# Performance work log

Hardware: AMD Instinct MI355X
Metric: run time of the kernel (lower is better)

## Reference

```python
import jax, jax.numpy as jnp
import numpy as np

T, B, I, H = 2048, 64, 256, 512

def _orthogonal(key, rows, cols):
    # mimic torch.nn.init.orthogonal_ semantics (QR of gaussian, sign-fixed)
    a = jax.random.normal(key, (max(rows, cols), min(rows, cols)), dtype=jnp.float32)
    q, r = jnp.linalg.qr(a)
    q = q * jnp.sign(jnp.diagonal(r))
    if rows < cols:
        q = q.T
    return q[:rows, :cols]

def setup_inputs() -> dict:
    key = jax.random.key(0)
    k1, k2, k3 = jax.random.split(key, 3)
    inp = jax.random.normal(k1, (T, B, I), dtype=jnp.float32)
    w_in = _orthogonal(k2, I, H)
    w_rec = _orthogonal(k3, H, H)
    return {"input": inp, "w_in": w_in, "w_rec": w_rec}

def reference(input, w_in, w_rec):
    # Precompute input projections for all timesteps in one big GEMM: [T,B,H]
    x_proj = jnp.einsum('tbi,ih->tbh', input, w_in)
    h0 = jnp.zeros((input.shape[1], w_rec.shape[0]), dtype=input.dtype)

    def step(h, xp_t):
        h_next = jnp.tanh(xp_t + h @ w_rec)
        return h_next, h_next

    h_last, hiddens = jax.lax.scan(step, h0, x_proj)
    return hiddens, h_last
```

## Files before the change

### kernel.cpp

```cpp
#include <hip/hip_runtime.h>

#define T_STEPS 2048
#define BATCH   64
#define IN_DIM  256
#define HID     512

typedef _Float16 half_t;
typedef half_t half2_t __attribute__((ext_vector_type(2)));

#if __has_builtin(__builtin_amdgcn_fdot2)
__device__ __forceinline__ float fdot2(half2_t a, half2_t b, float c) {
    return __builtin_amdgcn_fdot2(a, b, c, false);
}
#else
__device__ __forceinline__ float fdot2(half2_t a, half2_t b, float c) {
    return c + (float)a.x * (float)b.x + (float)a.y * (float)b.y;
}
#endif

struct alignas(16) h2x4 { half2_t v[4]; };

__global__ __launch_bounds__(256, 4)
void xproj_gemm(const float* __restrict__ A, const float* __restrict__ Win,
                float* __restrict__ out) {
    __shared__ float As[32][132];
    __shared__ float Bs[32][132];
    const int tid = threadIdx.x;
    const int m0 = blockIdx.y * 128;
    const int n0 = blockIdx.x * 128;
    const int tm = (tid >> 4) << 3;
    const int tn = (tid & 15) << 3;

    float acc[8][8] = {};

    for (int k0 = 0; k0 < IN_DIM; k0 += 32) {
        {
            const int m  = tid >> 3;
            const int k4 = (tid & 7) << 2;
#pragma unroll
            for (int r = 0; r < 4; ++r) {
                const float4 a4 = *(const float4*)&A[(size_t)(m0 + m + 32 * r) * IN_DIM + k0 + k4];
                As[k4 + 0][m + 32 * r] = a4.x;
                As[k4 + 1][m + 32 * r] = a4.y;
                As[k4 + 2][m + 32 * r] = a4.z;
                As[k4 + 3][m + 32 * r] = a4.w;
            }
        }
        {
            const int kb = tid >> 5;
            const int n4 = (tid & 31) << 2;
#pragma unroll
            for (int r = 0; r < 4; ++r) {
                const float4 b4 = *(const float4*)&Win[(size_t)(k0 + kb + 8 * r) * HID + n0 + n4];
                *(float4*)&Bs[kb + 8 * r][n4] = b4;
            }
        }
        __syncthreads();
#pragma unroll
        for (int kk = 0; kk < 32; ++kk) {
            const float4 a0 = *(const float4*)&As[kk][tm];
            const float4 a1 = *(const float4*)&As[kk][tm + 4];
            const float4 b0 = *(const float4*)&Bs[kk][tn];
            const float4 b1 = *(const float4*)&Bs[kk][tn + 4];
            const float av[8] = {a0.x, a0.y, a0.z, a0.w, a1.x, a1.y, a1.z, a1.w};
            const float bv[8] = {b0.x, b0.y, b0.z, b0.w, b1.x, b1.y, b1.z, b1.w};
#pragma unroll
            for (int i = 0; i < 8; ++i)
#pragma unroll
                for (int j = 0; j < 8; ++j)
                    acc[i][j] = fmaf(av[i], bv[j], acc[i][j]);
        }
        __syncthreads();
    }

#pragma unroll
    for (int i = 0; i < 8; ++i) {
        float4 c0 = {acc[i][0], acc[i][1], acc[i][2], acc[i][3]};
        float4 c1 = {acc[i][4], acc[i][5], acc[i][6], acc[i][7]};
        float* dst = &out[(size_t)(m0 + tm + i) * HID + n0 + tn];
        *(float4*)dst       = c0;
        *(float4*)(dst + 4) = c1;
    }
}

__global__ __attribute__((amdgpu_flat_work_group_size(512, 512),
                          amdgpu_waves_per_eu(2, 2)))
void rnn_scan(const float* __restrict__ Wrec, float* __restrict__ out) {
    __shared__ h2x4  WL4[16 * 512];
    __shared__ float parts[8 * 640];
    __shared__ h2x4  h4buf[64];

    const int tid   = threadIdx.x;
    const int b     = blockIdx.x;
    const int jg    = tid & 63;
    const int kg    = tid >> 6;
    const int col0  = jg << 3;
    const int kbase = kg << 6;

    half2_t wreg[8][24];
#pragma unroll
    for (int p = 0; p < 24; ++p) {
        const int k = kbase + 2 * p;
        const float4 lo0 = *(const float4*)&Wrec[(size_t)k * HID + col0];
        const float4 lo1 = *(const float4*)&Wrec[(size_t)k * HID + col0 + 4];
        const float4 hi0 = *(const float4*)&Wrec[(size_t)(k + 1) * HID + col0];
        const float4 hi1 = *(const float4*)&Wrec[(size_t)(k + 1) * HID + col0 + 4];
        wreg[0][p].x = (half_t)lo0.x; wreg[0][p].y = (half_t)hi0.x;
        wreg[1][p].x = (half_t)lo0.y; wreg[1][p].y = (half_t)hi0.y;
        wreg[2][p].x = (half_t)lo0.z; wreg[2][p].y = (half_t)hi0.z;
        wreg[3][p].x = (half_t)lo0.w; wreg[3][p].y = (half_t)hi0.w;
        wreg[4][p].x = (half_t)lo1.x; wreg[4][p].y = (half_t)hi1.x;
        wreg[5][p].x = (half_t)lo1.y; wreg[5][p].y = (half_t)hi1.y;
        wreg[6][p].x = (half_t)lo1.z; wreg[6][p].y = (half_t)hi1.z;
        wreg[7][p].x = (half_t)lo1.w; wreg[7][p].y = (half_t)hi1.w;
    }
#pragma unroll
    for (int q = 0; q < 2; ++q) {
        h2x4 bu[8];
#pragma unroll
        for (int pp = 0; pp < 4; ++pp) {
            const int k = kbase + 48 + 8 * q + 2 * pp;
            const float4 lo0 = *(const float4*)&Wrec[(size_t)k * HID + col0];
            const float4 lo1 = *(const float4*)&Wrec[(size_t)k * HID + col0 + 4];
            const float4 hi0 = *(const float4*)&Wrec[(size_t)(k + 1) * HID + col0];
            const float4 hi1 = *(const float4*)&Wrec[(size_t)(k + 1) * HID + col0 + 4];
            bu[0].v[pp].x = (half_t)lo0.x; bu[0].v[pp].y = (half_t)hi0.x;
            bu[1].v[pp].x = (half_t)lo0.y; bu[1].v[pp].y = (half_t)hi0.y;
            bu[2].v[pp].x = (half_t)lo0.z; bu[2].v[pp].y = (half_t)hi0.z;
            bu[3].v[pp].x = (half_t)lo0.w; bu[3].v[pp].y = (half_t)hi0.w;
            bu[4].v[pp].x = (half_t)lo1.x; bu[4].v[pp].y = (half_t)hi1.x;
            bu[5].v[pp].x = (half_t)lo1.y; bu[5].v[pp].y = (half_t)hi1.y;
            bu[6].v[pp].x = (half_t)lo1.z; bu[6].v[pp].y = (half_t)hi1.z;
            bu[7].v[pp].x = (half_t)lo1.w; bu[7].v[pp].y = (half_t)hi1.w;
        }
#pragma unroll
        for (int c = 0; c < 8; ++c)
            WL4[(c * 2 + q) * 512 + tid] = bu[c];
    }
    if (tid < 64) {
        h2x4 z;
        z.v[0] = half2_t{(half_t)0.f, (half_t)0.f};
        z.v[1] = z.v[0]; z.v[2] = z.v[0]; z.v[3] = z.v[0];
        h4buf[tid] = z;
    }
    __syncthreads();

    const int jcol  = tid;
    const int pbase = 9 * (jcol >> 3) + (jcol & 7);
    const h2x4* hbase = &h4buf[kg << 3];

    for (int t = 0; t < T_STEPS; ++t) {
        const float xpv = out[((size_t)t * BATCH + b) * HID + jcol];

        float acc[8] = {};

#pragma unroll
        for (int j = 0; j < 6; ++j) {
            const h2x4 hu = hbase[j];
#pragma unroll
            for (int pp = 0; pp < 4; ++pp)
#pragma unroll
                for (int c = 0; c < 8; ++c)
                    acc[c] = fdot2(wreg[c][4 * j + pp], hu.v[pp], acc[c]);
        }
#pragma unroll
        for (int q = 0; q < 2; ++q) {
            const h2x4 hu = hbase[6 + q];
#pragma unroll
            for (int c = 0; c < 8; ++c) {
                const h2x4 wu = WL4[(c * 2 + q) * 512 + tid];
#pragma unroll
                for (int pp = 0; pp < 4; ++pp)
                    acc[c] = fdot2(wu.v[pp], hu.v[pp], acc[c]);
            }
        }
#pragma unroll
        for (int c = 0; c < 8; ++c)
            parts[kg * 640 + 9 * jg + c] = acc[c];
        __syncthreads();

        float s = xpv;
#pragma unroll
        for (int g = 0; g < 8; ++g)
            s += parts[g * 640 + pbase];
        const float e  = __expf(2.0f * s);
        const float hj = 1.0f - 2.0f / (e + 1.0f);

        out[((size_t)t * BATCH + b) * HID + jcol] = hj;
        if (t == T_STEPS - 1)
            out[(size_t)T_STEPS * BATCH * HID + (size_t)b * HID + jcol] = hj;

        ((half_t*)h4buf)[jcol] = (half_t)hj;
        __syncthreads();
    }
}

extern "C" void kernel_launch(void* const* d_in, const int* in_sizes, int n_in,
                              void* d_out, int out_size, void* d_ws, size_t ws_size,
                              hipStream_t stream) {
    const float* A    = (const float*)d_in[0];
    const float* Win  = (const float*)d_in[1];
    const float* Wrec = (const float*)d_in[2];
    float* out = (float*)d_out;

    dim3 g1(HID / 128, (T_STEPS * BATCH) / 128);
    xproj_gemm<<<g1, 256, 0, stream>>>(A, Win, out);
    rnn_scan<<<BATCH, 512, 0, stream>>>(Wrec, out);
}
```

Measured before the change: 3.626 ms.

## Offload half of recurrent matvec to MFMA alongside fdot2 partial sums

The recurrent h@W_rec reduction is split in two. The upper 256 K-rows are computed with MFMA 16x16x32 f16 instructions, using B fragments held in registers and a broadcast h row, and only output row 0 is kept. The lower 256 K-rows still go through the fdot2 register/LDS path, now with half the per-thread work. The aim is to cut per-step VALU latency on the serial critical path by using the matrix cores, even though most of each MFMA tile is wasted and an extra LDS reduction buffer is added. The end-of-step __syncthreads is also replaced by an explicit lgkmcnt wait plus s_barrier.

Measured after the change: 4.620 ms. 1.27x slower.

```diff
diff --git a/kernel.cpp b/kernel.cpp
--- a/kernel.cpp
+++ b/kernel.cpp
@@ -7,6 +7,8 @@
 
 typedef _Float16 half_t;
 typedef half_t half2_t __attribute__((ext_vector_type(2)));
+typedef _Float16 f16x8 __attribute__((ext_vector_type(8)));
+typedef float f32x4 __attribute__((ext_vector_type(4)));
 
 #if __has_builtin(__builtin_amdgcn_fdot2)
 __device__ __forceinline__ float fdot2(half2_t a, half2_t b, float c) {
@@ -86,20 +88,23 @@
 __global__ __attribute__((amdgpu_flat_work_group_size(512, 512),
                           amdgpu_waves_per_eu(2, 2)))
 void rnn_scan(const float* __restrict__ Wrec, float* __restrict__ out) {
-    __shared__ h2x4  WL4[16 * 512];
+    __shared__ h2x4  WA[8 * 512];
+    __shared__ h2x4  WB[8 * 512];
     __shared__ float parts[8 * 640];
-    __shared__ h2x4  h4buf[64];
+    __shared__ float parts_m[512];
+    __shared__ f16x8 h2raw[64];
 
     const int tid   = threadIdx.x;
     const int b     = blockIdx.x;
     const int jg    = tid & 63;
     const int kg    = tid >> 6;
     const int col0  = jg << 3;
-    const int kbase = kg << 6;
-
-    half2_t wreg[8][24];
-#pragma unroll
-    for (int p = 0; p < 24; ++p) {
+    const int kbase = kg << 5;
+    const int lane  = tid & 63;
+
+    half2_t wreg[8][8];
+#pragma unroll
+    for (int p = 0; p < 8; ++p) {
         const int k = kbase + 2 * p;
         const float4 lo0 = *(const float4*)&Wrec[(size_t)k * HID + col0];
         const float4 lo1 = *(const float4*)&Wrec[(size_t)k * HID + col0 + 4];
@@ -119,7 +124,7 @@
         h2x4 bu[8];
 #pragma unroll
         for (int pp = 0; pp < 4; ++pp) {
-            const int k = kbase + 48 + 8 * q + 2 * pp;
+            const int k = kbase + 16 + 8 * q + 2 * pp;
             const float4 lo0 = *(const float4*)&Wrec[(size_t)k * HID + col0];
             const float4 lo1 = *(const float4*)&Wrec[(size_t)k * HID + col0 + 4];
             const float4 hi0 = *(const float4*)&Wrec[(size_t)(k + 1) * HID + col0];
@@ -133,53 +138,95 @@
             bu[6].v[pp].x = (half_t)lo1.z; bu[6].v[pp].y = (half_t)hi1.z;
             bu[7].v[pp].x = (half_t)lo1.w; bu[7].v[pp].y = (half_t)hi1.w;
         }
+        h2x4* slab = q ? WB : WA;
 #pragma unroll
         for (int c = 0; c < 8; ++c)
-            WL4[(c * 2 + q) * 512 + tid] = bu[c];
-    }
+            slab[c * 512 + tid] = bu[c];
+    }
+    const int lrow = tid & 15;
+    const int lgrp = (tid >> 4) & 3;
+    f16x8 bfrag[4][8];
+#pragma unroll
+    for (int tl = 0; tl < 4; ++tl)
+#pragma unroll
+        for (int K = 0; K < 8; ++K) {
+            const int col = (kg << 6) + (tl << 4) + lrow;
+            const int kb  = 256 + (K << 5) + (lgrp << 3);
+            f16x8 f;
+#pragma unroll
+            for (int i = 0; i < 8; ++i)
+                f[i] = (half_t)Wrec[(size_t)(kb + i) * HID + col];
+            bfrag[tl][K] = f;
+        }
     if (tid < 64) {
-        h2x4 z;
-        z.v[0] = half2_t{(half_t)0.f, (half_t)0.f};
-        z.v[1] = z.v[0]; z.v[2] = z.v[0]; z.v[3] = z.v[0];
-        h4buf[tid] = z;
+        f16x8 z;
+#pragma unroll
+        for (int i = 0; i < 8; ++i) z[i] = (half_t)0.f;
+        h2raw[tid] = z;
     }
     __syncthreads();
 
-    const int jcol  = tid;
-    const int pbase = 9 * (jcol >> 3) + (jcol & 7);
-    const h2x4* hbase = &h4buf[kg << 3];
+    const h2x4* hb4  = (const h2x4*)h2raw;
+    const int jcol   = tid;
+    const int pbase  = 9 * (jcol >> 3) + (jcol & 7);
 
     for (int t = 0; t < T_STEPS; ++t) {
         const float xpv = out[((size_t)t * BATCH + b) * HID + jcol];
 
+        f32x4 d0 = {0.f, 0.f, 0.f, 0.f};
+        f32x4 d1 = d0, d2 = d0, d3 = d0;
+#pragma unroll
+        for (int K = 0; K < 8; ++K) {
+            const f16x8 af = h2raw[32 + (K << 2) + lgrp];
+            d0 = __builtin_amdgcn_mfma_f32_16x16x32_f16(af, bfrag[0][K], d0, 0, 0, 0);
+            d1 = __builtin_amdgcn_mfma_f32_16x16x32_f16(af, bfrag[1][K], d1, 0, 0, 0);
+            d2 = __builtin_amdgcn_mfma_f32_16x16x32_f16(af, bfrag[2][K], d2, 0, 0, 0);
+            d3 = __builtin_amdgcn_mfma_f32_16x16x32_f16(af, bfrag[3][K], d3, 0, 0, 0);
+        }
+
         float acc[8] = {};
-
-#pragma unroll
-        for (int j = 0; j < 6; ++j) {
-            const h2x4 hu = hbase[j];
+#pragma unroll
+        for (int j = 0; j < 2; ++j) {
+            const h2x4 hu = hb4[(kg << 2) + j];
 #pragma unroll
             for (int pp = 0; pp < 4; ++pp)
 #pragma unroll
                 for (int c = 0; c < 8; ++c)
                     acc[c] = fdot2(wreg[c][4 * j + pp], hu.v[pp], acc[c]);
         }
-#pragma unroll
-        for (int q = 0; q < 2; ++q) {
-            const h2x4 hu = hbase[6 + q];
+        {
+            const h2x4 hu = hb4[(kg << 2) + 2];
 #pragma unroll
             for (int c = 0; c < 8; ++c) {
-                const h2x4 wu = WL4[(c * 2 + q) * 512 + tid];
+                const h2x4 wu = WA[c * 512 + tid];
 #pragma unroll
                 for (int pp = 0; pp < 4; ++pp)
                     acc[c] = fdot2(wu.v[pp], hu.v[pp], acc[c]);
             }
         }
+        {
+            const h2x4 hu = hb4[(kg << 2) + 3];
+#pragma unroll
+            for (int c = 0; c < 8; ++c) {
+                const h2x4 wu = WB[c * 512 + tid];
+#pragma unroll
+                for (int pp = 0; pp < 4; ++pp)
+                    acc[c] = fdot2(wu.v[pp], hu.v[pp], acc[c]);
+            }
+        }
+
 #pragma unroll
         for (int c = 0; c < 8; ++c)
             parts[kg * 640 + 9 * jg + c] = acc[c];
+        if (lane < 16) {
+            parts_m[(kg << 6) +  0 + lane] = d0[0];
+            parts_m[(kg << 6) + 16 + lane] = d1[0];
+            parts_m[(kg << 6) + 32 + lane] = d2[0];
+            parts_m[(kg << 6) + 48 + lane] = d3[0];
+        }
         __syncthreads();
 
-        float s = xpv;
+        float s = xpv + parts_m[jcol];
 #pragma unroll
         for (int g = 0; g < 8; ++g)
             s += parts[g * 640 + pbase];
@@ -190,8 +237,9 @@
         if (t == T_STEPS - 1)
             out[(size_t)T_STEPS * BATCH * HID + (size_t)b * HID + jcol] = hj;
 
-        ((half_t*)h4buf)[jcol] = (half_t)hj;
-        __syncthreads();
+        ((half_t*)h2raw)[jcol] = (half_t)hj;
+        asm volatile("s_waitcnt lgkmcnt(0)" ::: "memory");
+        __builtin_amdgcn_s_barrier();
     }
 }
 
```
